# Optimization experiments

Hardware: AMD Instinct MI355X
Metric: run time of the kernel (lower is better)

The kernel has to match this reference:

```python
import jax, jax.numpy as jnp
import numpy as np

B, S, D = 4, 2048, 1024
H, DH = 16, 64
SCALE = DH ** -0.5


def setup_inputs() -> dict:
    key = jax.random.key(0)
    ks = jax.random.split(key, 7)
    x_q = jax.random.normal(ks[0], (B, S, D), dtype=jnp.float32)
    x_k = jax.random.normal(ks[1], (B, S, D), dtype=jnp.float32)
    x_v = jax.random.normal(ks[2], (B, S, D), dtype=jnp.float32)
    # causal mask: True means masked (matches torch masked_fill semantics)
    mask = jnp.triu(jnp.ones((S, S), dtype=bool), k=1)
    # Linear init: randn(in, out) / sqrt(out), no bias
    Wq = jax.random.normal(ks[3], (D, H * DH), dtype=jnp.float32) / np.sqrt(H * DH)
    Wk = jax.random.normal(ks[4], (D, H * DH), dtype=jnp.float32) / np.sqrt(H * DH)
    Wv = jax.random.normal(ks[5], (D, H * DH), dtype=jnp.float32) / np.sqrt(H * DH)
    Wo = jax.random.normal(ks[6], (H * DH, D), dtype=jnp.float32) / np.sqrt(D)
    return {"x_q": x_q, "x_k": x_k, "x_v": x_v, "mask": mask,
            "Wq": Wq, "Wk": Wk, "Wv": Wv, "Wo": Wo}


def reference(x_q, x_k, x_v, mask, Wq, Wk, Wv, Wo):
    def split_heads(x):  # [B,S,H*DH] -> [B,H,S,DH]
        return x.reshape(B, S, H, DH).transpose(0, 2, 1, 3)

    q = split_heads(x_q @ Wq)
    k = split_heads(x_k @ Wk)
    v = split_heads(x_v @ Wv)
    attn = jnp.einsum('bhqd,bhkd->bhqk', q, k) * SCALE
    attn = jnp.where(mask, -jnp.inf, attn)
    w_attn = jax.nn.softmax(attn, axis=-1)  # dropout p=0.0 is identity
    out = jnp.einsum('bhqk,bhkd->bhqd', w_attn, v)
    out = out.transpose(0, 2, 1, 3).reshape(B, S, H * DH)
    return out @ Wo
```

## Files before the change

kernel.cpp:

```cpp
#include <hip/hip_runtime.h>
#include <hip/hip_bf16.h>
#include <math.h>

#define BB 4
#define SS 2048
#define DD 1024
#define HH 16
#define DHE 64
#define NH (HH*DHE)
constexpr float NEG_BIG = -1e30f;

typedef __bf16 bf16x8 __attribute__((ext_vector_type(8)));
typedef float  f32x4  __attribute__((ext_vector_type(4)));

#define WAITVM6()   asm volatile("s_waitcnt vmcnt(6)" ::: "memory")
#define WAITVM4()   asm volatile("s_waitcnt vmcnt(4)" ::: "memory")
#define WAITVM0()   asm volatile("s_waitcnt vmcnt(0)" ::: "memory")
#define WAITLGKM0() asm volatile("s_waitcnt lgkmcnt(0)" ::: "memory")
#define MEMFENCE()  asm volatile("" ::: "memory")

__device__ __forceinline__ void gl_lds16(const __bf16* g, __bf16* l) {
  __builtin_amdgcn_global_load_lds(
      (const __attribute__((address_space(1))) unsigned int*)g,
      (__attribute__((address_space(3))) unsigned int*)l, 16, 0, 0);
}

__device__ __forceinline__ unsigned pack_bf2(float lo, float hi) {
  union { __bf16 h[2]; unsigned u; } p;
  p.h[0] = (__bf16)lo; p.h[1] = (__bf16)hi;
  return p.u;
}

__global__ __launch_bounds__(256) void wtrans_k(
    const float* __restrict__ w0, const float* __restrict__ w1,
    const float* __restrict__ w2, const float* __restrict__ w3,
    __bf16* __restrict__ o0, __bf16* __restrict__ o1,
    __bf16* __restrict__ o2, __bf16* __restrict__ o3) {
  __shared__ __bf16 t[32][33];
  const float* w = blockIdx.z == 0 ? w0 : blockIdx.z == 1 ? w1 : blockIdx.z == 2 ? w2 : w3;
  __bf16*      o = blockIdx.z == 0 ? o0 : blockIdx.z == 1 ? o1 : blockIdx.z == 2 ? o2 : o3;
  int tx = threadIdx.x & 31, ty = threadIdx.x >> 5;
  int bk = blockIdx.x * 32, bn = blockIdx.y * 32;
  #pragma unroll
  for (int i = 0; i < 4; i++)
    t[ty + i * 8][tx] = (__bf16)w[(size_t)(bk + ty + i * 8) * DD + bn + tx];
  __syncthreads();
  #pragma unroll
  for (int i = 0; i < 4; i++)
    o[(size_t)(bn + ty + i * 8) * DD + bk + tx] = t[tx][ty + i * 8];
}

__global__ __launch_bounds__(256) void vtrans_k(
    const __bf16* __restrict__ v, __bf16* __restrict__ o) {
  __shared__ __bf16 t[32][33];
  int tx = threadIdx.x & 31, ty = threadIdx.x >> 5;
  int bs = blockIdx.x * 32, bc = blockIdx.y * 32;
  const __bf16* vz = v + (size_t)blockIdx.z * SS * NH;
  __bf16*       oz = o + (size_t)blockIdx.z * NH * SS;
  #pragma unroll
  for (int i = 0; i < 4; i++)
    t[ty + i * 8][tx] = vz[(size_t)(bs + ty + i * 8) * NH + bc + tx];
  __syncthreads();
  #pragma unroll
  for (int i = 0; i < 4; i++)
    oz[(size_t)(bc + ty + i * 8) * SS + bs + tx] = t[tx][ty + i * 8];
}

struct B3 {
  const void*  a0; const void*  a1; const void*  a2;
  const __bf16* b0; const __bf16* b1; const __bf16* b2;
  void* c0; void* c1; void* c2;
};

template <typename AT> struct AStage;
template <> struct AStage<float>  { f32x4 d[2][2]; };
template <> struct AStage<__bf16> { bf16x8 d[2]; };

template <typename AT, typename CT>
__global__ __launch_bounds__(256, 3) void gemm_bt(B3 p, size_t aoff) {
  __shared__ __bf16 As[128][40];
  __shared__ __bf16 Bs[4][128][32];

  const unsigned nwg  = gridDim.x * gridDim.y * gridDim.z;
  const unsigned flat = blockIdx.x + gridDim.x * (blockIdx.y + gridDim.y * blockIdx.z);
  const unsigned swz  = (flat & 7) * (nwg >> 3) + (flat >> 3);
  const int bx = swz % gridDim.x;
  const unsigned rem = swz / gridDim.x;
  const int by = rem % gridDim.y;
  const int z  = rem / gridDim.y;

  const AT* __restrict__ A =
      (const AT*)(z == 0 ? p.a0 : z == 1 ? p.a1 : p.a2);
  const __bf16* __restrict__ BT = z == 0 ? p.b0 : z == 1 ? p.b1 : p.b2;
  CT* __restrict__ C = (CT*)(z == 0 ? p.c0 : z == 1 ? p.c1 : p.c2);

  const int tid  = threadIdx.x;
  const int wave = tid >> 6, lane = tid & 63;
  const int quad = lane >> 4, l16 = lane & 15;
  const int wr = (wave >> 1) * 64, wc = (wave & 1) * 64;
  const int m0 = by * 128, n0 = bx * 128;

  f32x4 acc[4][4] = {};
  AStage<AT> aA, aB;

  auto loadA = [&](int k0, AStage<AT>& S) {
    #pragma unroll
    for (int i = 0; i < 2; i++) {
      int c = tid + i * 256;
      int row = c >> 2, seg = (c & 3) * 8;
      if constexpr (sizeof(AT) == 4) {
        const float* ap = (const float*)A + aoff + (size_t)(m0 + row) * DD + k0 + seg;
        S.d[i][0] = *(const f32x4*)ap;
        S.d[i][1] = *(const f32x4*)(ap + 4);
      } else {
        S.d[i] = *(const bf16x8*)((const __bf16*)A + aoff + (size_t)(m0 + row) * DD + k0 + seg);
      }
    }
  };
  auto issueB = [&](int k0, int buf) {
    #pragma unroll
    for (int i = 0; i < 2; i++) {
      int rr  = lane >> 2;
      int row = wave * 16 + i * 64 + rr;
      int seg = (lane & 3) ^ ((rr >> 1) & 3);
      gl_lds16(&BT[(size_t)(n0 + row) * DD + k0 + seg * 8],
               &Bs[buf][wave * 16 + i * 64][0]);
    }
  };

  auto step = [&](int it, AStage<AT>& S, bool last, bool tail) {
    if (last) { WAITVM0(); }
    else if constexpr (sizeof(AT) == 4) { WAITVM6(); }
    else { WAITVM4(); }
    __builtin_amdgcn_s_barrier();
    #pragma unroll
    for (int i = 0; i < 2; i++) {
      int c = tid + i * 256;
      bf16x8 av;
      if constexpr (sizeof(AT) == 4) {
        #pragma unroll
        for (int j = 0; j < 4; j++) {
          av[j]     = (__bf16)S.d[i][0][j];
          av[j + 4] = (__bf16)S.d[i][1][j];
        }
      } else {
        av = S.d[i];
      }
      *(bf16x8*)&As[c >> 2][(c & 3) * 8] = av;
    }
    WAITLGKM0();
    __builtin_amdgcn_s_barrier();
    if (!tail) {
      issueB((it + 2) * 32, (it + 2) & 3);
      loadA((it + 2) * 32, S);
    }
    const int buf = it & 3;
    bf16x8 af[4], bfr[4];
    #pragma unroll
    for (int t = 0; t < 4; t++) {
      af[t]  = *(const bf16x8*)&As[wr + t * 16 + l16][quad * 8];
      bfr[t] = *(const bf16x8*)&Bs[buf][wc + t * 16 + l16][(quad ^ ((l16 >> 1) & 3)) * 8];
    }
    __builtin_amdgcn_s_setprio(1);
    #pragma unroll
    for (int mt = 0; mt < 4; mt++)
      #pragma unroll
      for (int nt = 0; nt < 4; nt++)
        acc[mt][nt] = __builtin_amdgcn_mfma_f32_16x16x32_bf16(af[mt], bfr[nt], acc[mt][nt], 0, 0, 0);
    __builtin_amdgcn_s_setprio(0);
  };

  issueB(0, 0);  loadA(0, aA);
  MEMFENCE();
  issueB(32, 1); loadA(32, aB);
  MEMFENCE();

  for (int it2 = 0; it2 < 15; it2++) {
    step(2 * it2,     aA, false, false);
    step(2 * it2 + 1, aB, false, false);
  }
  step(30, aA, false, true);
  step(31, aB, true,  true);

  #pragma unroll
  for (int mt = 0; mt < 4; mt++)
    #pragma unroll
    for (int nt = 0; nt < 4; nt++)
      #pragma unroll
      for (int r = 0; r < 4; r++) {
        int row = m0 + wr + mt * 16 + quad * 4 + r;
        int col = n0 + wc + nt * 16 + l16;
        C[(size_t)row * NH + col] = (CT)acc[mt][nt][r];
      }
}

__global__ __launch_bounds__(256, 4) void attn_k(
    const __bf16* __restrict__ Q, const __bf16* __restrict__ K,
    const __bf16* __restrict__ VT, __bf16* __restrict__ O) {
  __shared__ __bf16 Ks[64][68];
  __shared__ __bf16 Vs[64][68];

  const int tid  = threadIdx.x;
  const int wave = tid >> 6, lane = tid & 63;
  const int quad = lane >> 4, l16 = lane & 15;

  const int n    = blockIdx.x;
  const int xcd  = n & 7, slot = n >> 3;
  const int gidx = xcd + 8 * (slot >> 4);
  const int bx   = slot & 15;
  const int h = gidx & 15, z = gidx >> 4;

  const __bf16* Qg = Q + (size_t)z * SS * NH + h * DHE;
  const __bf16* Kg = K + (size_t)z * SS * NH + h * DHE;
  const __bf16* Vg = VT + ((size_t)z * HH + h) * DHE * SS;
  __bf16*       Og = O + (size_t)z * SS * NH + h * DHE;

  bf16x8 kreg[2], vreg[2];
  auto loadKV = [&](int k0) {
    #pragma unroll
    for (int i = 0; i < 2; i++) {
      int v = tid + i * 256;
      kreg[i] = *(const bf16x8*)&Kg[(size_t)(k0 + (v >> 3)) * NH + (v & 7) * 8];
      vreg[i] = *(const bf16x8*)&Vg[(size_t)(v >> 3) * SS + k0 + (v & 7) * 8];
    }
  };

  #pragma unroll 1
  for (int seg = 0; seg < 2; seg++) {
    const int qt = seg ? bx : 31 - bx;
    const int q0 = qt * 64;
    const int ntiles = qt + 1;

    const int qrow = q0 + wave * 16 + l16;
    bf16x8 qf[2];
    #pragma unroll
    for (int kk = 0; kk < 2; kk++) {
      bf16x8 t = *(const bf16x8*)&Qg[(size_t)qrow * NH + kk * 32 + quad * 8];
      #pragma unroll
      for (int j = 0; j < 8; j++) t[j] = (__bf16)((float)t[j] * 0.125f);
      qf[kk] = t;
    }

    loadKV(0);
    float prows = 0.f;
    f32x4 oacc[4] = {};

    for (int kt = 0; kt < ntiles; kt++) {
      const int k0 = kt * 64;
      __syncthreads();
      #pragma unroll
      for (int i = 0; i < 2; i++) {
        int v = tid + i * 256;
        *(bf16x8*)&Ks[v >> 3][(v & 7) * 8] = kreg[i];
        *(bf16x8*)&Vs[v >> 3][(v & 7) * 8] = vreg[i];
      }
      __syncthreads();
      if (kt + 1 < ntiles) loadKV(k0 + 64);

      const bool diag = (kt == ntiles - 1);
      const int nq  = diag ? wave + 1 : 4;
      const int nsm = diag ? ((wave + 2) & ~1) : 4;
      const int nkk = nsm >> 1;

      f32x4 sc[4] = {};
      __builtin_amdgcn_s_setprio(1);
      #pragma unroll
      for (int kk = 0; kk < 2; kk++)
        #pragma unroll
        for (int nt = 0; nt < 4; nt++)
          if (nt < nq) {
            bf16x8 kf = *(const bf16x8*)&Ks[nt * 16 + l16][kk * 32 + quad * 8];
            sc[nt] = __builtin_amdgcn_mfma_f32_16x16x32_bf16(kf, qf[kk], sc[nt], 0, 0, 0);
          }
      __builtin_amdgcn_s_setprio(0);

      bf16x8 pf[2];
      #pragma unroll
      for (int t = 0; t < 2; t++)
        if (t < nkk) {
          const int nt0 = 2 * t, nt1 = 2 * t + 1;
          float pA[4], pB[4];
          #pragma unroll
          for (int r = 0; r < 4; r++) {
            float v0 = sc[nt0][r], v1 = sc[nt1][r];
            if (diag) {
              const int kb = k0 + quad * 4 + r;
              if (kb + nt0 * 16 > qrow) v0 = NEG_BIG;
              if (kb + nt1 * 16 > qrow) v1 = NEG_BIG;
            }
            pA[r] = __expf(v0); pB[r] = __expf(v1);
            prows += pA[r] + pB[r];
          }
          unsigned a0 = pack_bf2(pA[0], pA[1]), a1 = pack_bf2(pA[2], pA[3]);
          unsigned b0 = pack_bf2(pB[0], pB[1]), b1 = pack_bf2(pB[2], pB[3]);
          unsigned x0 = (quad & 1) ? a0 : b0, x1 = (quad & 1) ? a1 : b1;
          unsigned y0 = (quad & 1) ? b0 : a0, y1 = (quad & 1) ? b1 : a1;
          unsigned r16_0 = __shfl_xor((int)x0, 16), r16_1 = __shfl_xor((int)x1, 16);
          unsigned r32_0 = __shfl_xor((int)x0, 32), r32_1 = __shfl_xor((int)x1, 32);
          unsigned r48_0 = __shfl_xor((int)y0, 48), r48_1 = __shfl_xor((int)y1, 48);
          unsigned w0 = quad == 0 ? a0    : quad == 1 ? r48_0 : quad == 2 ? r32_0 : r16_0;
          unsigned w1 = quad == 0 ? a1    : quad == 1 ? r48_1 : quad == 2 ? r32_1 : r16_1;
          unsigned w2 = quad == 0 ? r16_0 : quad == 1 ? r32_0 : quad == 2 ? r48_0 : b0;
          unsigned w3 = quad == 0 ? r16_1 : quad == 1 ? r32_1 : quad == 2 ? r48_1 : b1;
          union { unsigned u[4]; bf16x8 v; } asm_;
          asm_.u[0] = w0; asm_.u[1] = w1; asm_.u[2] = w2; asm_.u[3] = w3;
          pf[t] = asm_.v;
        }

      __builtin_amdgcn_s_setprio(1);
      #pragma unroll
      for (int kk = 0; kk < 2; kk++)
        if (kk < nkk) {
          #pragma unroll
          for (int dt = 0; dt < 4; dt++) {
            bf16x8 vf = *(const bf16x8*)&Vs[dt * 16 + l16][kk * 32 + quad * 8];
            oacc[dt] = __builtin_amdgcn_mfma_f32_16x16x32_bf16(pf[kk], vf, oacc[dt], 0, 0, 0);
          }
        }
      __builtin_amdgcn_s_setprio(0);
    }

    prows += __shfl_xor(prows, 16, 64);
    prows += __shfl_xor(prows, 32, 64);

    #pragma unroll
    for (int r = 0; r < 4; r++) {
      float tot = __shfl(prows, quad * 4 + r, 64);
      float inv = tot > 0.f ? 1.0f / tot : 0.f;
      int qg = q0 + wave * 16 + quad * 4 + r;
      #pragma unroll
      for (int dt = 0; dt < 4; dt++)
        Og[(size_t)qg * NH + dt * 16 + l16] = (__bf16)(oacc[dt][r] * inv);
    }
  }
}

extern "C" void kernel_launch(void* const* d_in, const int* in_sizes, int n_in,
                              void* d_out, int out_size, void* d_ws, size_t ws_size,
                              hipStream_t stream) {
  const float* x_q = (const float*)d_in[0];
  const float* x_k = (const float*)d_in[1];
  const float* x_v = (const float*)d_in[2];
  const float* Wq = (const float*)d_in[4];
  const float* Wk = (const float*)d_in[5];
  const float* Wv = (const float*)d_in[6];
  const float* Wo = (const float*)d_in[7];
  float* out = (float*)d_out;

  const size_t WTE = (size_t)DD * NH;
  const size_t PB  = (size_t)SS * NH;
  const size_t FULLB = (size_t)BB * PB;

  char* ws = (char*)d_ws;
  __bf16* WqT = (__bf16*)ws;
  __bf16* WkT = WqT + WTE;
  __bf16* WvT = WkT + WTE;
  __bf16* WoT = WvT + WTE;
  __bf16* buf0 = WoT + WTE;

  wtrans_k<<<dim3(32, 32, 4), 256, 0, stream>>>(Wq, Wk, Wv, Wo, WqT, WkT, WvT, WoT);

  const size_t needFull = 4 * WTE * 2 + 4 * FULLB * 2;
  if (ws_size >= needFull) {
    __bf16* Qb = buf0;
    __bf16* Kb = Qb + FULLB;
    __bf16* Vb = Kb + FULLB;
    __bf16* VT = Vb + FULLB;
    __bf16* Ob = Vb;
    B3 qkv = { x_q, x_k, x_v, WqT, WkT, WvT, Qb, Kb, Vb };
    gemm_bt<float, __bf16><<<dim3(8, 64, 3), 256, 0, stream>>>(qkv, 0);
    vtrans_k<<<dim3(SS / 32, NH / 32, BB), 256, 0, stream>>>(Vb, VT);
    attn_k<<<dim3((SS / 128) * HH * BB), 256, 0, stream>>>(Qb, Kb, VT, Ob);
    B3 og = { Ob, Ob, Ob, WoT, WoT, WoT, out, out, out };
    gemm_bt<__bf16, float><<<dim3(8, 64, 1), 256, 0, stream>>>(og, 0);
  } else {
    __bf16* Qb = buf0;
    __bf16* Kb = Qb + PB;
    __bf16* Vb = Kb + PB;
    __bf16* VT = Vb + PB;
    __bf16* Ob = Vb;
    for (int b = 0; b < BB; b++) {
      const size_t boff = (size_t)b * PB;
      B3 qkv = { x_q, x_k, x_v, WqT, WkT, WvT, Qb, Kb, Vb };
      gemm_bt<float, __bf16><<<dim3(8, 16, 3), 256, 0, stream>>>(qkv, boff);
      vtrans_k<<<dim3(SS / 32, NH / 32, 1), 256, 0, stream>>>(Vb, VT);
      attn_k<<<dim3((SS / 128) * HH), 256, 0, stream>>>(Qb, Kb, VT, Ob);
      B3 og = { Ob, Ob, Ob, WoT, WoT, WoT, out + boff, out + boff, out + boff };
      gemm_bt<__bf16, float><<<dim3(8, 16, 1), 256, 0, stream>>>(og, 0);
    }
  }
}
```

Before: 350.5 us.

## Pre-convert activations to bf16 and use triple-buffered direct-to-LDS GEMM

Adds a conversion kernel that casts the fp32 x_q/x_k/x_v inputs to bf16 in workspace. It also adds a new GEMM kernel that streams both A and B tiles straight into LDS with global_load_lds, using a 3-slot ring buffer and XOR-swizzled layout. The aim is to remove register staging and fp32 conversion from the GEMM inner loop and overlap loads with MFMA work. The cost is an extra full pass over the inputs and more workspace, with a fallback to the old path when the workspace is too small.

```diff
diff --git a/kernel.cpp b/kernel.cpp
--- a/kernel.cpp
+++ b/kernel.cpp
@@ -29,6 +29,24 @@
   union { __bf16 h[2]; unsigned u; } p;
   p.h[0] = (__bf16)lo; p.h[1] = (__bf16)hi;
   return p.u;
+}
+
+__global__ __launch_bounds__(256) void cvt_k(
+    const float* __restrict__ x0, const float* __restrict__ x1,
+    const float* __restrict__ x2,
+    __bf16* __restrict__ o0, __bf16* __restrict__ o1, __bf16* __restrict__ o2) {
+  const float* x = blockIdx.z == 0 ? x0 : blockIdx.z == 1 ? x1 : x2;
+  __bf16*      o = blockIdx.z == 0 ? o0 : blockIdx.z == 1 ? o1 : o2;
+  const size_t n8 = (size_t)BB * SS * DD / 8;
+  for (size_t i = (size_t)blockIdx.x * 256 + threadIdx.x; i < n8;
+       i += (size_t)gridDim.x * 256) {
+    f32x4 a = *(const f32x4*)(x + i * 8);
+    f32x4 b = *(const f32x4*)(x + i * 8 + 4);
+    bf16x8 v;
+    #pragma unroll
+    for (int j = 0; j < 4; j++) { v[j] = (__bf16)a[j]; v[j + 4] = (__bf16)b[j]; }
+    *(bf16x8*)(o + i * 8) = v;
+  }
 }
 
 __global__ __launch_bounds__(256) void wtrans_k(
@@ -72,14 +90,10 @@
   void* c0; void* c1; void* c2;
 };
 
-template <typename AT> struct AStage;
-template <> struct AStage<float>  { f32x4 d[2][2]; };
-template <> struct AStage<__bf16> { bf16x8 d[2]; };
-
-template <typename AT, typename CT>
-__global__ __launch_bounds__(256, 3) void gemm_bt(B3 p, size_t aoff) {
-  __shared__ __bf16 As[128][40];
-  __shared__ __bf16 Bs[4][128][32];
+template <typename CT>
+__global__ __launch_bounds__(256, 3) void gemm_bb(B3 p) {
+  __shared__ __bf16 Asr[3][128][32];
+  __shared__ __bf16 Bsr[3][128][32];
 
   const unsigned nwg  = gridDim.x * gridDim.y * gridDim.z;
   const unsigned flat = blockIdx.x + gridDim.x * (blockIdx.y + gridDim.y * blockIdx.z);
@@ -89,8 +103,93 @@
   const int by = rem % gridDim.y;
   const int z  = rem / gridDim.y;
 
-  const AT* __restrict__ A =
-      (const AT*)(z == 0 ? p.a0 : z == 1 ? p.a1 : p.a2);
+  const __bf16* __restrict__ A  = (const __bf16*)(z == 0 ? p.a0 : z == 1 ? p.a1 : p.a2);
+  const __bf16* __restrict__ BT = z == 0 ? p.b0 : z == 1 ? p.b1 : p.b2;
+  CT* __restrict__ C = (CT*)(z == 0 ? p.c0 : z == 1 ? p.c1 : p.c2);
+
+  const int tid  = threadIdx.x;
+  const int wave = tid >> 6, lane = tid & 63;
+  const int quad = lane >> 4, l16 = lane & 15;
+  const int wr = (wave >> 1) * 64, wc = (wave & 1) * 64;
+  const int m0 = by * 128, n0 = bx * 128;
+
+  f32x4 acc[4][4] = {};
+
+  auto issue = [&](int it, int slot) {
+    const int k0 = it * 32;
+    const int rr  = lane >> 2;
+    const int seg = (lane & 3) ^ ((rr >> 1) & 3);
+    #pragma unroll
+    for (int i = 0; i < 2; i++) {
+      const int row = wave * 16 + i * 64 + rr;
+      gl_lds16(&A [(size_t)(m0 + row) * DD + k0 + seg * 8], &Asr[slot][wave * 16 + i * 64][0]);
+      gl_lds16(&BT[(size_t)(n0 + row) * DD + k0 + seg * 8], &Bsr[slot][wave * 16 + i * 64][0]);
+    }
+  };
+
+  auto compute = [&](int s) {
+    bf16x8 af[4], bfr[4];
+    const int ph = (quad ^ ((l16 >> 1) & 3)) * 8;
+    #pragma unroll
+    for (int t = 0; t < 4; t++) {
+      af[t]  = *(const bf16x8*)&Asr[s][wr + t * 16 + l16][ph];
+      bfr[t] = *(const bf16x8*)&Bsr[s][wc + t * 16 + l16][ph];
+    }
+    __builtin_amdgcn_s_setprio(1);
+    #pragma unroll
+    for (int mt = 0; mt < 4; mt++)
+      #pragma unroll
+      for (int nt = 0; nt < 4; nt++)
+        acc[mt][nt] = __builtin_amdgcn_mfma_f32_16x16x32_bf16(af[mt], bfr[nt], acc[mt][nt], 0, 0, 0);
+    __builtin_amdgcn_s_setprio(0);
+  };
+
+  issue(0, 0); MEMFENCE();
+  issue(1, 1); MEMFENCE();
+
+  int cur = 0, pre = 2;
+  #pragma unroll 1
+  for (int it = 0; it < 30; it++) {
+    WAITVM4();
+    __builtin_amdgcn_s_barrier();
+    issue(it + 2, pre);
+    compute(cur);
+    cur = cur == 2 ? 0 : cur + 1;
+    pre = pre == 2 ? 0 : pre + 1;
+  }
+  WAITVM4(); __builtin_amdgcn_s_barrier(); compute(cur);
+  cur = cur == 2 ? 0 : cur + 1;
+  WAITVM0(); __builtin_amdgcn_s_barrier(); compute(cur);
+
+  #pragma unroll
+  for (int mt = 0; mt < 4; mt++)
+    #pragma unroll
+    for (int nt = 0; nt < 4; nt++)
+      #pragma unroll
+      for (int r = 0; r < 4; r++) {
+        int row = m0 + wr + mt * 16 + quad * 4 + r;
+        int col = n0 + wc + nt * 16 + l16;
+        C[(size_t)row * NH + col] = (CT)acc[mt][nt][r];
+      }
+}
+
+template <typename AT> struct AStage;
+template <> struct AStage<float>  { f32x4 d[2][2]; };
+template <> struct AStage<__bf16> { bf16x8 d[2]; };
+
+template <typename AT, typename CT>
+__global__ __launch_bounds__(256, 3) void gemm_bt(B3 p, size_t aoff) {
+  __shared__ __bf16 As[128][40];
+  __shared__ __bf16 Bs[4][128][32];
+  const unsigned nwg  = gridDim.x * gridDim.y * gridDim.z;
+  const unsigned flat = blockIdx.x + gridDim.x * (blockIdx.y + gridDim.y * blockIdx.z);
+  const unsigned swz  = (flat & 7) * (nwg >> 3) + (flat >> 3);
+  const int bx = swz % gridDim.x;
+  const unsigned rem = swz / gridDim.x;
+  const int by = rem % gridDim.y;
+  const int z  = rem / gridDim.y;
+
+  const AT* __restrict__ A = (const AT*)(z == 0 ? p.a0 : z == 1 ? p.a1 : p.a2);
   const __bf16* __restrict__ BT = z == 0 ? p.b0 : z == 1 ? p.b1 : p.b2;
   CT* __restrict__ C = (CT*)(z == 0 ? p.c0 : z == 1 ? p.c1 : p.c2);
 
@@ -360,8 +459,25 @@
 
   wtrans_k<<<dim3(32, 32, 4), 256, 0, stream>>>(Wq, Wk, Wv, Wo, WqT, WkT, WvT, WoT);
 
+  const size_t needFast = 4 * WTE * 2 + 4 * FULLB * 2 + 3 * FULLB * 2;
   const size_t needFull = 4 * WTE * 2 + 4 * FULLB * 2;
-  if (ws_size >= needFull) {
+  if (ws_size >= needFast) {
+    __bf16* Qb  = buf0;
+    __bf16* Kb  = Qb + FULLB;
+    __bf16* Vb  = Kb + FULLB;
+    __bf16* VT  = Vb + FULLB;
+    __bf16* xqb = VT + FULLB;
+    __bf16* xkb = xqb + FULLB;
+    __bf16* xvb = xkb + FULLB;
+    __bf16* Ob  = Vb;
+    cvt_k<<<dim3(1024, 1, 3), 256, 0, stream>>>(x_q, x_k, x_v, xqb, xkb, xvb);
+    B3 qkv = { xqb, xkb, xvb, WqT, WkT, WvT, Qb, Kb, Vb };
+    gemm_bb<__bf16><<<dim3(8, 64, 3), 256, 0, stream>>>(qkv);
+    vtrans_k<<<dim3(SS / 32, NH / 32, BB), 256, 0, stream>>>(Vb, VT);
+    attn_k<<<dim3((SS / 128) * HH * BB), 256, 0, stream>>>(Qb, Kb, VT, Ob);
+    B3 og = { Ob, Ob, Ob, WoT, WoT, WoT, out, out, out };
+    gemm_bb<float><<<dim3(8, 64, 1), 256, 0, stream>>>(og);
+  } else if (ws_size >= needFull) {
     __bf16* Qb = buf0;
     __bf16* Kb = Qb + FULLB;
     __bf16* Vb = Kb + FULLB;
```

New measurement: 334.2 us. -4.6%, faster.
